# Kernel optimization log

Hardware: AMD Instinct MI355X
Metric: run time of the kernel (lower is better)

Reference implementation:

```python
import jax, jax.numpy as jnp
import numpy as np

NUM_HEADS = 12

def setup_inputs() -> dict:
    key = jax.random.key(0)
    ks = jax.random.split(key, 6)
    B, N, C, P = 16, 785, 768, 48
    return {
        "x": jax.random.normal(ks[0], (B, N, C), jnp.float32),
        "qkv_w": jax.random.normal(ks[1], (3 * C, C), jnp.float32) * 0.02,
        "pos_emb": jax.random.normal(ks[2], (N, N, P), jnp.float32) * 0.02,
        "pos_proj_w": jax.random.normal(ks[3], (NUM_HEADS, P), jnp.float32) * 0.02,
        "proj_w": jax.random.normal(ks[4], (C, C), jnp.float32) * 0.02,
        "proj_b": jnp.zeros((C,), jnp.float32),
    }

def reference(x, qkv_w, pos_emb, pos_proj_w, proj_w, proj_b):
    B, N, C = x.shape
    H = NUM_HEADS
    hd = C // H
    scale = hd ** -0.5
    # qkv projection: [B,N,3C] -> q,k,v each [B,H,N,hd]
    qkv = (x @ qkv_w.T).reshape(B, N, 3, H, hd)
    qkv = jnp.transpose(qkv, (2, 0, 3, 1, 4))
    q, k, v = qkv[0], qkv[1], qkv[2]
    # learned relative-position bias: [H,N,N]
    pos_score = jnp.einsum('nmp,hp->hnm', pos_emb, pos_proj_w)
    # attention scores: scale applied AFTER adding bias (matches original)
    attn = (jnp.einsum('bhnd,bhmd->bhnm', q, k) + pos_score[None]) * scale
    attn = jax.nn.softmax(attn, axis=-1)
    out = jnp.einsum('bhnm,bhmd->bhnd', attn, v)
    out = jnp.transpose(out, (0, 2, 1, 3)).reshape(B, N, C)
    return out @ proj_w.T + proj_b
```

## Files before the change

### kernel.cpp

```cpp
#include <hip/hip_runtime.h>
#include <hip/hip_fp16.h>

#define B_ 16
#define N_ 785
#define C_ 768
#define H_ 12
#define HD_ 64
#define P_ 48
#define M_ (B_*N_)
#define MPAD 12672
#define POSW 800
#define VTW  800
#define SCALE 0.125f

#define OFF_Q   0
#define OFF_K   9646080
#define OFF_VT  19292160
#define OFF_POS 29122560
#define OFF_XF  36658560
#define OFF_AO  OFF_XF
#define OFF_WQ  46390656
#define OFF_WP  48160128

struct __align__(16) Half8 { __half h[8]; };
typedef _Float16 half8_t __attribute__((ext_vector_type(8)));
typedef _Float16 half4_t __attribute__((ext_vector_type(4)));
typedef float f32x4 __attribute__((ext_vector_type(4)));

__device__ __forceinline__ void gl16(const void* g, void* l) {
    __builtin_amdgcn_global_load_lds(
        (const __attribute__((address_space(1))) void*)g,
        (__attribute__((address_space(3))) void*)l, 16, 0, 0);
}

#define NX4 2411520
#define NQ4 442368
#define NP4 147456
#define NTOT4 (NX4+NQ4+NP4)

__global__ __launch_bounds__(256) void convert_f16(
    const float* __restrict__ x, const float* __restrict__ wq,
    const float* __restrict__ wp, _Float16* __restrict__ xo,
    _Float16* __restrict__ wqo, _Float16* __restrict__ wpo)
{
    int i = blockIdx.x * 256 + threadIdx.x;
    const float4* s; _Float16* d; int o;
    if (i < NX4)            { s = (const float4*)x;  d = xo;  o = i; }
    else if (i < NX4 + NQ4) { s = (const float4*)wq; d = wqo; o = i - NX4; }
    else                    { s = (const float4*)wp; d = wpo; o = i - NX4 - NQ4; }
    float4 v = s[o];
    half4_t h = { (_Float16)v.x, (_Float16)v.y, (_Float16)v.z, (_Float16)v.w };
    *(half4_t*)&d[o * 4] = h;
}

__global__ __launch_bounds__(256) void qkv_gemm_mfma(
    const _Float16* __restrict__ A, const _Float16* __restrict__ Bw,
    __half* __restrict__ qh, __half* __restrict__ kh, __half* __restrict__ vth)
{
    __shared__ _Float16 Asl[128 * 32];
    __shared__ _Float16 Bsl[128 * 32];

    const int t  = threadIdx.x;
    const int w  = t >> 6;
    const int l  = t & 63;
    const int lr = l & 15;
    const int lg = l >> 4;
    const int wm = (w >> 1) * 64;
    const int wn = (w & 1) * 64;
    const int n0 = blockIdx.x * 128;
    const int m0 = blockIdx.y * 128;

    const int f1 = t + 256;
    const int ar0 = t >> 2,  ac0 = (t & 3) * 8;
    const int ar1 = f1 >> 2, ac1 = (f1 & 3) * 8;
    const _Float16* Ag0 = A  + (size_t)(m0 + ar0) * 768 + ac0;
    const _Float16* Ag1 = A  + (size_t)(m0 + ar1) * 768 + ac1;
    const _Float16* Bg0 = Bw + (size_t)(n0 + ar0) * 768 + ac0;
    const _Float16* Bg1 = Bw + (size_t)(n0 + ar1) * 768 + ac1;
    _Float16* Al0 = &Asl[t * 8];
    _Float16* Al1 = &Asl[f1 * 8];
    _Float16* Bl0 = &Bsl[t * 8];
    _Float16* Bl1 = &Bsl[f1 * 8];

    f32x4 acc[4][4];
    #pragma unroll
    for (int i = 0; i < 4; ++i)
        #pragma unroll
        for (int j = 0; j < 4; ++j) acc[i][j] = (f32x4){0.f, 0.f, 0.f, 0.f};

    for (int k0 = 0; k0 < 768; k0 += 32) {
        gl16(Ag0 + k0, Al0); gl16(Ag1 + k0, Al1);
        gl16(Bg0 + k0, Bl0); gl16(Bg1 + k0, Bl1);
        __syncthreads();
        half8_t af[4], bf[4];
        #pragma unroll
        for (int i = 0; i < 4; ++i)
            af[i] = *(const half8_t*)&Asl[(wm + i * 16 + lr) * 32 + lg * 8];
        #pragma unroll
        for (int j = 0; j < 4; ++j)
            bf[j] = *(const half8_t*)&Bsl[(wn + j * 16 + lr) * 32 + lg * 8];
        #pragma unroll
        for (int i = 0; i < 4; ++i)
            #pragma unroll
            for (int j = 0; j < 4; ++j)
                acc[i][j] = __builtin_amdgcn_mfma_f32_16x16x32_f16(af[i], bf[j], acc[i][j], 0, 0, 0);
        __syncthreads();
    }

    const int tsel  = blockIdx.x / 6;
    const int nbase = n0 - tsel * 768;
    #pragma unroll
    for (int i = 0; i < 4; ++i) {
        #pragma unroll
        for (int r = 0; r < 4; ++r) {
            const int m = m0 + wm + i * 16 + lg * 4 + r;
            if (m >= M_) continue;
            const int bb = m / N_, nn = m - bb * N_;
            #pragma unroll
            for (int j = 0; j < 4; ++j) {
                const int nsec = nbase + wn + j * 16 + lr;
                const int hh = nsec >> 6, dd = nsec & 63;
                const float v = acc[i][j][r];
                if (tsel == 0)
                    qh[((size_t)(bb * H_ + hh) * N_ + nn) * HD_ + dd] = __float2half(v * SCALE);
                else if (tsel == 1)
                    kh[((size_t)(bb * H_ + hh) * N_ + nn) * HD_ + dd] = __float2half(v);
                else
                    vth[((size_t)(bb * H_ + hh) * HD_ + dd) * VTW + nn] = __float2half(v);
            }
        }
    }
}

__global__ __launch_bounds__(256) void pos_kernel(
    const float* __restrict__ pe, const float* __restrict__ pw,
    __half* __restrict__ posh)
{
    __shared__ float W[H_][P_];
    const int t = threadIdx.x;
    for (int i = t; i < H_ * P_; i += 256) W[i / P_][i % P_] = pw[i];
    __syncthreads();
    int nm = blockIdx.x * 256 + t;
    if (nm >= N_ * N_) return;
    float e[48];
    const float4* src = (const float4*)(pe + (size_t)nm * 48);
    #pragma unroll
    for (int i = 0; i < 12; ++i) {
        float4 v = src[i];
        e[4*i] = v.x; e[4*i+1] = v.y; e[4*i+2] = v.z; e[4*i+3] = v.w;
    }
    int n = nm / N_, m = nm - n * N_;
    #pragma unroll
    for (int hh = 0; hh < H_; ++hh) {
        float s = 0.f;
        #pragma unroll
        for (int p = 0; p < 48; ++p) s = fmaf(e[p], W[hh][p], s);
        posh[((size_t)hh * N_ + n) * POSW + m] = __float2half(s * SCALE);
    }
}

__global__ __launch_bounds__(256) void attn_mfma(
    const _Float16* __restrict__ qh, const _Float16* __restrict__ kh,
    const _Float16* __restrict__ vt, const _Float16* __restrict__ posh,
    _Float16* __restrict__ aoh)
{
    __shared__ _Float16 Kl[64][72];
    __shared__ _Float16 Vl[64][72];
    __shared__ _Float16 Bl[64][72];
    __shared__ _Float16 Pl[4][16][72];

    const int t  = threadIdx.x;
    const int w  = t >> 6;
    const int l  = t & 63;
    const int lr = l & 15;
    const int lg = l >> 4;
    const int bh = blockIdx.y;
    const int h  = bh % H_;
    const int n0 = blockIdx.x * 64;

    const int qrow = n0 + w * 16 + lr;
    const int qrc  = qrow < N_ ? qrow : N_ - 1;
    const half8_t qf0 = *(const half8_t*)(qh + ((size_t)bh * N_ + qrc) * HD_ + lg * 8);
    const half8_t qf1 = *(const half8_t*)(qh + ((size_t)bh * N_ + qrc) * HD_ + 32 + lg * 8);

    f32x4 O0 = {0.f,0.f,0.f,0.f}, O1 = O0, O2 = O0, O3 = O0;
    float mr[4] = {-1e30f, -1e30f, -1e30f, -1e30f};
    float ls[4] = {0.f, 0.f, 0.f, 0.f};

    const int srow = t >> 2;
    const int scol = (t & 3) * 16;

    for (int c = 0; c < 13; ++c) {
        const int m0 = c * 64;
        {
            const int gm = (m0 + srow) < N_ ? (m0 + srow) : N_ - 1;
            const half8_t* ksrc = (const half8_t*)(kh + ((size_t)bh * N_ + gm) * HD_ + scol);
            *(half8_t*)&Kl[srow][scol]     = ksrc[0];
            *(half8_t*)&Kl[srow][scol + 8] = ksrc[1];
            const half8_t* vsrc = (const half8_t*)(vt + ((size_t)bh * HD_ + srow) * VTW + m0 + scol);
            *(half8_t*)&Vl[srow][scol]     = vsrc[0];
            *(half8_t*)&Vl[srow][scol + 8] = vsrc[1];
            const int gn = (n0 + srow) < N_ ? (n0 + srow) : N_ - 1;
            const half8_t* bsrc = (const half8_t*)(posh + ((size_t)h * N_ + gn) * POSW + m0 + scol);
            *(half8_t*)&Bl[srow][scol]     = bsrc[0];
            *(half8_t*)&Bl[srow][scol + 8] = bsrc[1];
        }
        __syncthreads();

        f32x4 s[4];
        #pragma unroll
        for (int ms = 0; ms < 4; ++ms) {
            half8_t k0 = *(const half8_t*)&Kl[ms * 16 + lr][lg * 8];
            half8_t k1 = *(const half8_t*)&Kl[ms * 16 + lr][32 + lg * 8];
            f32x4 acc = {0.f, 0.f, 0.f, 0.f};
            acc = __builtin_amdgcn_mfma_f32_16x16x32_f16(qf0, k0, acc, 0, 0, 0);
            acc = __builtin_amdgcn_mfma_f32_16x16x32_f16(qf1, k1, acc, 0, 0, 0);
            s[ms] = acc;
        }
        #pragma unroll
        for (int ms = 0; ms < 4; ++ms) {
            const bool valid = (m0 + ms * 16 + lr) < N_;
            #pragma unroll
            for (int r = 0; r < 4; ++r) {
                float b = (float)Bl[w * 16 + lg * 4 + r][ms * 16 + lr];
                s[ms][r] = valid ? (s[ms][r] + b) : -1e30f;
            }
        }
        float alpha[4];
        #pragma unroll
        for (int r = 0; r < 4; ++r) {
            float v = fmaxf(fmaxf(s[0][r], s[1][r]), fmaxf(s[2][r], s[3][r]));
            v = fmaxf(v, __shfl_xor(v, 1));
            v = fmaxf(v, __shfl_xor(v, 2));
            v = fmaxf(v, __shfl_xor(v, 4));
            v = fmaxf(v, __shfl_xor(v, 8));
            float mn = fmaxf(mr[r], v);
            alpha[r] = __expf(mr[r] - mn);
            mr[r] = mn;
        }
        float psum[4] = {0.f, 0.f, 0.f, 0.f};
        #pragma unroll
        for (int ms = 0; ms < 4; ++ms) {
            #pragma unroll
            for (int r = 0; r < 4; ++r) {
                float p = __expf(s[ms][r] - mr[r]);
                psum[r] += p;
                Pl[w][lg * 4 + r][ms * 16 + lr] = (_Float16)p;
            }
        }
        #pragma unroll
        for (int r = 0; r < 4; ++r) {
            float v = psum[r];
            v += __shfl_xor(v, 1);
            v += __shfl_xor(v, 2);
            v += __shfl_xor(v, 4);
            v += __shfl_xor(v, 8);
            ls[r] = ls[r] * alpha[r] + v;
            O0[r] *= alpha[r]; O1[r] *= alpha[r];
            O2[r] *= alpha[r]; O3[r] *= alpha[r];
        }
        const half8_t pa0 = *(const half8_t*)&Pl[w][lr][lg * 8];
        const half8_t pa1 = *(const half8_t*)&Pl[w][lr][32 + lg * 8];
        #pragma unroll
        for (int ds = 0; ds < 4; ++ds) {
            half8_t v0 = *(const half8_t*)&Vl[ds * 16 + lr][lg * 8];
            half8_t v1 = *(const half8_t*)&Vl[ds * 16 + lr][32 + lg * 8];
            f32x4& Od = (ds == 0 ? O0 : ds == 1 ? O1 : ds == 2 ? O2 : O3);
            Od = __builtin_amdgcn_mfma_f32_16x16x32_f16(pa0, v0, Od, 0, 0, 0);
            Od = __builtin_amdgcn_mfma_f32_16x16x32_f16(pa1, v1, Od, 0, 0, 0);
        }
        __syncthreads();
    }

    const int bb = bh / H_;
    #pragma unroll
    for (int r = 0; r < 4; ++r) {
        const int n = n0 + w * 16 + lg * 4 + r;
        if (n >= N_) continue;
        const float inv = 1.f / ls[r];
        _Float16* dst = aoh + ((size_t)(bb * N_ + n)) * C_ + h * HD_;
        dst[0 * 16 + lr] = (_Float16)(O0[r] * inv);
        dst[1 * 16 + lr] = (_Float16)(O1[r] * inv);
        dst[2 * 16 + lr] = (_Float16)(O2[r] * inv);
        dst[3 * 16 + lr] = (_Float16)(O3[r] * inv);
    }
}

__global__ __launch_bounds__(256) void proj_gemm_mfma(
    const _Float16* __restrict__ A, const _Float16* __restrict__ Bw,
    const float* __restrict__ bias, float* __restrict__ out)
{
    __shared__ _Float16 Asl[128 * 32];
    __shared__ _Float16 Bsl[128 * 32];

    const int t  = threadIdx.x;
    const int w  = t >> 6;
    const int l  = t & 63;
    const int lr = l & 15;
    const int lg = l >> 4;
    const int wm = (w >> 1) * 64;
    const int wn = (w & 1) * 64;
    const int n0 = blockIdx.x * 128;
    const int m0 = blockIdx.y * 128;

    const int f1 = t + 256;
    const int ar0 = t >> 2,  ac0 = (t & 3) * 8;
    const int ar1 = f1 >> 2, ac1 = (f1 & 3) * 8;
    const _Float16* Ag0 = A  + (size_t)(m0 + ar0) * 768 + ac0;
    const _Float16* Ag1 = A  + (size_t)(m0 + ar1) * 768 + ac1;
    const _Float16* Bg0 = Bw + (size_t)(n0 + ar0) * 768 + ac0;
    const _Float16* Bg1 = Bw + (size_t)(n0 + ar1) * 768 + ac1;
    _Float16* Al0 = &Asl[t * 8];
    _Float16* Al1 = &Asl[f1 * 8];
    _Float16* Bl0 = &Bsl[t * 8];
    _Float16* Bl1 = &Bsl[f1 * 8];

    f32x4 acc[4][4];
    #pragma unroll
    for (int i = 0; i < 4; ++i)
        #pragma unroll
        for (int j = 0; j < 4; ++j) acc[i][j] = (f32x4){0.f, 0.f, 0.f, 0.f};

    for (int k0 = 0; k0 < 768; k0 += 32) {
        gl16(Ag0 + k0, Al0); gl16(Ag1 + k0, Al1);
        gl16(Bg0 + k0, Bl0); gl16(Bg1 + k0, Bl1);
        __syncthreads();
        half8_t af[4], bf[4];
        #pragma unroll
        for (int i = 0; i < 4; ++i)
            af[i] = *(const half8_t*)&Asl[(wm + i * 16 + lr) * 32 + lg * 8];
        #pragma unroll
        for (int j = 0; j < 4; ++j)
            bf[j] = *(const half8_t*)&Bsl[(wn + j * 16 + lr) * 32 + lg * 8];
        #pragma unroll
        for (int i = 0; i < 4; ++i)
            #pragma unroll
            for (int j = 0; j < 4; ++j)
                acc[i][j] = __builtin_amdgcn_mfma_f32_16x16x32_f16(af[i], bf[j], acc[i][j], 0, 0, 0);
        __syncthreads();
    }

    float bj[4];
    #pragma unroll
    for (int j = 0; j < 4; ++j) bj[j] = bias[n0 + wn + j * 16 + lr];
    #pragma unroll
    for (int i = 0; i < 4; ++i) {
        #pragma unroll
        for (int r = 0; r < 4; ++r) {
            const int m = m0 + wm + i * 16 + lg * 4 + r;
            if (m >= M_) continue;
            #pragma unroll
            for (int j = 0; j < 4; ++j) {
                const int n = n0 + wn + j * 16 + lr;
                out[(size_t)m * 768 + n] = acc[i][j][r] + bj[j];
            }
        }
    }
}

extern "C" void kernel_launch(void* const* d_in, const int* in_sizes, int n_in,
                              void* d_out, int out_size, void* d_ws, size_t ws_size,
                              hipStream_t stream)
{
    const float* x     = (const float*)d_in[0];
    const float* qkv_w = (const float*)d_in[1];
    const float* pe    = (const float*)d_in[2];
    const float* pw    = (const float*)d_in[3];
    const float* pjw   = (const float*)d_in[4];
    const float* pjb   = (const float*)d_in[5];
    float* out = (float*)d_out;

    _Float16* wsh  = (_Float16*)d_ws;
    _Float16* qh   = wsh + OFF_Q;
    _Float16* kh   = wsh + OFF_K;
    _Float16* vth  = wsh + OFF_VT;
    _Float16* posh = wsh + OFF_POS;
    _Float16* xf   = wsh + OFF_XF;
    _Float16* aoh  = wsh + OFF_AO;
    _Float16* wqf  = wsh + OFF_WQ;
    _Float16* wpf  = wsh + OFF_WP;

    convert_f16<<<dim3(NTOT4 / 256), 256, 0, stream>>>(x, qkv_w, pjw, xf, wqf, wpf);
    qkv_gemm_mfma<<<dim3(18, 99), 256, 0, stream>>>(
        xf, wqf, (__half*)qh, (__half*)kh, (__half*)vth);
    pos_kernel<<<dim3((N_ * N_ + 255) / 256), 256, 0, stream>>>(pe, pw, (__half*)posh);
    attn_mfma<<<dim3(13, 192), 256, 0, stream>>>(qh, kh, vth, posh, aoh);
    proj_gemm_mfma<<<dim3(6, 99), 256, 0, stream>>>(aoh, wpf, pjb, out);
}
```

Before: 312.4 us.

## Restructure attention loop with register prefetch, transposed scores, exp2 and lazy rescale

The attention kernel now computes S transposed (K as the A operand), so probabilities land in registers already laid out as the A fragment for the PV MFMA. This removes the per-wave shared-memory P buffer and its round trip. The next K/V/bias tile is prefetched into registers while the current one is computed, and the softmax uses exp2 with log2e folded into the Q and pos-bias scale. The running max is only updated when it grows by more than 8, and s_setprio is raised around MFMA blocks in all GEMMs. The grid is flattened so batch varies fastest, which puts blocks that share the same pos-bias tile next to each other for L2 reuse. The cost is more register pressure, and the lazy rescale leans on fp32 headroom (p can reach 2^8 before rescaling).

```diff
diff --git a/kernel.cpp b/kernel.cpp
--- a/kernel.cpp
+++ b/kernel.cpp
@@ -8,19 +8,18 @@
 #define HD_ 64
 #define P_ 48
 #define M_ (B_*N_)
-#define MPAD 12672
-#define POSW 800
-#define VTW  800
-#define SCALE 0.125f
+#define POSW 832
+#define VTW  832
+#define SLOG2E 0.1803368801111244f
 
 #define OFF_Q   0
 #define OFF_K   9646080
 #define OFF_VT  19292160
-#define OFF_POS 29122560
-#define OFF_XF  36658560
+#define OFF_POS 29515776
+#define OFF_XF  37353216
 #define OFF_AO  OFF_XF
-#define OFF_WQ  46390656
-#define OFF_WP  48160128
+#define OFF_WQ  47085312
+#define OFF_WP  48854784
 
 struct __align__(16) Half8 { __half h[8]; };
 typedef _Float16 half8_t __attribute__((ext_vector_type(8)));
@@ -99,11 +98,13 @@
         #pragma unroll
         for (int j = 0; j < 4; ++j)
             bf[j] = *(const half8_t*)&Bsl[(wn + j * 16 + lr) * 32 + lg * 8];
+        __builtin_amdgcn_s_setprio(1);
         #pragma unroll
         for (int i = 0; i < 4; ++i)
             #pragma unroll
             for (int j = 0; j < 4; ++j)
                 acc[i][j] = __builtin_amdgcn_mfma_f32_16x16x32_f16(af[i], bf[j], acc[i][j], 0, 0, 0);
+        __builtin_amdgcn_s_setprio(0);
         __syncthreads();
     }
 
@@ -122,7 +123,7 @@
                 const int hh = nsec >> 6, dd = nsec & 63;
                 const float v = acc[i][j][r];
                 if (tsel == 0)
-                    qh[((size_t)(bb * H_ + hh) * N_ + nn) * HD_ + dd] = __float2half(v * SCALE);
+                    qh[((size_t)(bb * H_ + hh) * N_ + nn) * HD_ + dd] = __float2half(v * SLOG2E);
                 else if (tsel == 1)
                     kh[((size_t)(bb * H_ + hh) * N_ + nn) * HD_ + dd] = __float2half(v);
                 else
@@ -155,7 +156,7 @@
         float s = 0.f;
         #pragma unroll
         for (int p = 0; p < 48; ++p) s = fmaf(e[p], W[hh][p], s);
-        posh[((size_t)hh * N_ + n) * POSW + m] = __float2half(s * SCALE);
+        posh[((size_t)hh * N_ + n) * POSW + m] = __float2half(s * SLOG2E);
     }
 }
 
@@ -167,108 +168,152 @@
     __shared__ _Float16 Kl[64][72];
     __shared__ _Float16 Vl[64][72];
     __shared__ _Float16 Bl[64][72];
-    __shared__ _Float16 Pl[4][16][72];
 
     const int t  = threadIdx.x;
     const int w  = t >> 6;
     const int l  = t & 63;
     const int lr = l & 15;
     const int lg = l >> 4;
-    const int bh = blockIdx.y;
-    const int h  = bh % H_;
-    const int n0 = blockIdx.x * 64;
+
+    const int g   = blockIdx.x;
+    const int b   = g & 15;
+    const int grp = g >> 4;
+    const int qt  = grp / 12;
+    const int h   = grp - qt * 12;
+    const int bh  = b * H_ + h;
+    const int n0  = qt * 64;
 
     const int qrow = n0 + w * 16 + lr;
     const int qrc  = qrow < N_ ? qrow : N_ - 1;
-    const half8_t qf0 = *(const half8_t*)(qh + ((size_t)bh * N_ + qrc) * HD_ + lg * 8);
-    const half8_t qf1 = *(const half8_t*)(qh + ((size_t)bh * N_ + qrc) * HD_ + 32 + lg * 8);
+    const _Float16* qbase = qh + ((size_t)bh * N_ + qrc) * HD_;
+    const half8_t qf0 = *(const half8_t*)(qbase + lg * 8);
+    const half8_t qf1 = *(const half8_t*)(qbase + 32 + lg * 8);
 
     f32x4 O0 = {0.f,0.f,0.f,0.f}, O1 = O0, O2 = O0, O3 = O0;
-    float mr[4] = {-1e30f, -1e30f, -1e30f, -1e30f};
-    float ls[4] = {0.f, 0.f, 0.f, 0.f};
+    float m_run = -1e30f;
+    float l_run = 0.f;
 
     const int srow = t >> 2;
     const int scol = (t & 3) * 16;
+    const _Float16* kRow = kh + ((size_t)bh * N_) * HD_ + scol;
+    const _Float16* vRow = vt + ((size_t)bh * HD_ + srow) * VTW + scol;
+    const _Float16* bRow = posh + ((size_t)h * N_ + (n0 + srow < N_ ? n0 + srow : N_ - 1)) * POSW + scol;
+
+    half8_t rk0, rk1, rv0, rv1, rb0, rb1;
+    {
+        const int gm = srow < N_ ? srow : N_ - 1;
+        const half8_t* ks = (const half8_t*)(kRow + (size_t)gm * HD_);
+        rk0 = ks[0]; rk1 = ks[1];
+        const half8_t* vs = (const half8_t*)vRow;
+        rv0 = vs[0]; rv1 = vs[1];
+        const half8_t* bs = (const half8_t*)bRow;
+        rb0 = bs[0]; rb1 = bs[1];
+    }
 
     for (int c = 0; c < 13; ++c) {
-        const int m0 = c * 64;
-        {
-            const int gm = (m0 + srow) < N_ ? (m0 + srow) : N_ - 1;
-            const half8_t* ksrc = (const half8_t*)(kh + ((size_t)bh * N_ + gm) * HD_ + scol);
-            *(half8_t*)&Kl[srow][scol]     = ksrc[0];
-            *(half8_t*)&Kl[srow][scol + 8] = ksrc[1];
-            const half8_t* vsrc = (const half8_t*)(vt + ((size_t)bh * HD_ + srow) * VTW + m0 + scol);
-            *(half8_t*)&Vl[srow][scol]     = vsrc[0];
-            *(half8_t*)&Vl[srow][scol + 8] = vsrc[1];
-            const int gn = (n0 + srow) < N_ ? (n0 + srow) : N_ - 1;
-            const half8_t* bsrc = (const half8_t*)(posh + ((size_t)h * N_ + gn) * POSW + m0 + scol);
-            *(half8_t*)&Bl[srow][scol]     = bsrc[0];
-            *(half8_t*)&Bl[srow][scol + 8] = bsrc[1];
-        }
-        __syncthreads();
+        *(half8_t*)&Kl[srow][scol]     = rk0;
+        *(half8_t*)&Kl[srow][scol + 8] = rk1;
+        *(half8_t*)&Vl[srow][scol]     = rv0;
+        *(half8_t*)&Vl[srow][scol + 8] = rv1;
+        *(half8_t*)&Bl[srow][scol]     = rb0;
+        *(half8_t*)&Bl[srow][scol + 8] = rb1;
+        __syncthreads();
+
+        if (c < 12) {
+            const int m0n = (c + 1) * 64;
+            const int gm  = (m0n + srow) < N_ ? (m0n + srow) : N_ - 1;
+            const half8_t* ks = (const half8_t*)(kRow + (size_t)gm * HD_);
+            rk0 = ks[0]; rk1 = ks[1];
+            const half8_t* vs = (const half8_t*)(vRow + m0n);
+            rv0 = vs[0]; rv1 = vs[1];
+            const half8_t* bs = (const half8_t*)(bRow + m0n);
+            rb0 = bs[0]; rb1 = bs[1];
+        }
 
         f32x4 s[4];
+        __builtin_amdgcn_s_setprio(1);
         #pragma unroll
         for (int ms = 0; ms < 4; ++ms) {
             half8_t k0 = *(const half8_t*)&Kl[ms * 16 + lr][lg * 8];
             half8_t k1 = *(const half8_t*)&Kl[ms * 16 + lr][32 + lg * 8];
             f32x4 acc = {0.f, 0.f, 0.f, 0.f};
-            acc = __builtin_amdgcn_mfma_f32_16x16x32_f16(qf0, k0, acc, 0, 0, 0);
-            acc = __builtin_amdgcn_mfma_f32_16x16x32_f16(qf1, k1, acc, 0, 0, 0);
+            acc = __builtin_amdgcn_mfma_f32_16x16x32_f16(k0, qf0, acc, 0, 0, 0);
+            acc = __builtin_amdgcn_mfma_f32_16x16x32_f16(k1, qf1, acc, 0, 0, 0);
             s[ms] = acc;
         }
+        __builtin_amdgcn_s_setprio(0);
+
         #pragma unroll
         for (int ms = 0; ms < 4; ++ms) {
-            const bool valid = (m0 + ms * 16 + lr) < N_;
+            half4_t b4 = *(const half4_t*)&Bl[w * 16 + lr][ms * 16 + lg * 4];
+            s[ms][0] += (float)b4[0];
+            s[ms][1] += (float)b4[1];
+            s[ms][2] += (float)b4[2];
+            s[ms][3] += (float)b4[3];
+        }
+        if (c == 12) {
+            #pragma unroll
+            for (int ms = 0; ms < 4; ++ms)
+                #pragma unroll
+                for (int r = 0; r < 4; ++r)
+                    if (ms * 16 + lg * 4 + r >= 17) s[ms][r] = -1e30f;
+        }
+
+        float smax = fmaxf(fmaxf(fmaxf(s[0][0], s[0][1]), fmaxf(s[0][2], s[0][3])),
+                           fmaxf(fmaxf(s[1][0], s[1][1]), fmaxf(s[1][2], s[1][3])));
+        smax = fmaxf(smax, fmaxf(fmaxf(fmaxf(s[2][0], s[2][1]), fmaxf(s[2][2], s[2][3])),
+                                 fmaxf(fmaxf(s[3][0], s[3][1]), fmaxf(s[3][2], s[3][3]))));
+        smax = fmaxf(smax, __shfl_xor(smax, 16));
+        smax = fmaxf(smax, __shfl_xor(smax, 32));
+
+        if (__any(smax > m_run + 8.f)) {
+            const float mn    = fmaxf(m_run, smax);
+            const float alpha = exp2f(m_run - mn);
+            m_run = mn;
+            l_run *= alpha;
+            const float a0 = __shfl(alpha, lg * 4 + 0);
+            const float a1 = __shfl(alpha, lg * 4 + 1);
+            const float a2 = __shfl(alpha, lg * 4 + 2);
+            const float a3 = __shfl(alpha, lg * 4 + 3);
+            O0[0]*=a0; O0[1]*=a1; O0[2]*=a2; O0[3]*=a3;
+            O1[0]*=a0; O1[1]*=a1; O1[2]*=a2; O1[3]*=a3;
+            O2[0]*=a0; O2[1]*=a1; O2[2]*=a2; O2[3]*=a3;
+            O3[0]*=a0; O3[1]*=a1; O3[2]*=a2; O3[3]*=a3;
+        }
+
+        float p[4][4];
+        float psum = 0.f;
+        #pragma unroll
+        for (int ms = 0; ms < 4; ++ms)
             #pragma unroll
             for (int r = 0; r < 4; ++r) {
-                float b = (float)Bl[w * 16 + lg * 4 + r][ms * 16 + lr];
-                s[ms][r] = valid ? (s[ms][r] + b) : -1e30f;
+                p[ms][r] = exp2f(s[ms][r] - m_run);
+                psum += p[ms][r];
             }
-        }
-        float alpha[4];
-        #pragma unroll
-        for (int r = 0; r < 4; ++r) {
-            float v = fmaxf(fmaxf(s[0][r], s[1][r]), fmaxf(s[2][r], s[3][r]));
-            v = fmaxf(v, __shfl_xor(v, 1));
-            v = fmaxf(v, __shfl_xor(v, 2));
-            v = fmaxf(v, __shfl_xor(v, 4));
-            v = fmaxf(v, __shfl_xor(v, 8));
-            float mn = fmaxf(mr[r], v);
-            alpha[r] = __expf(mr[r] - mn);
-            mr[r] = mn;
-        }
-        float psum[4] = {0.f, 0.f, 0.f, 0.f};
-        #pragma unroll
-        for (int ms = 0; ms < 4; ++ms) {
-            #pragma unroll
-            for (int r = 0; r < 4; ++r) {
-                float p = __expf(s[ms][r] - mr[r]);
-                psum[r] += p;
-                Pl[w][lg * 4 + r][ms * 16 + lr] = (_Float16)p;
-            }
-        }
-        #pragma unroll
-        for (int r = 0; r < 4; ++r) {
-            float v = psum[r];
-            v += __shfl_xor(v, 1);
-            v += __shfl_xor(v, 2);
-            v += __shfl_xor(v, 4);
-            v += __shfl_xor(v, 8);
-            ls[r] = ls[r] * alpha[r] + v;
-            O0[r] *= alpha[r]; O1[r] *= alpha[r];
-            O2[r] *= alpha[r]; O3[r] *= alpha[r];
-        }
-        const half8_t pa0 = *(const half8_t*)&Pl[w][lr][lg * 8];
-        const half8_t pa1 = *(const half8_t*)&Pl[w][lr][32 + lg * 8];
+        psum += __shfl_xor(psum, 16);
+        psum += __shfl_xor(psum, 32);
+        l_run += psum;
+
+        half8_t pa0 = { (_Float16)p[0][0], (_Float16)p[0][1], (_Float16)p[0][2], (_Float16)p[0][3],
+                        (_Float16)p[1][0], (_Float16)p[1][1], (_Float16)p[1][2], (_Float16)p[1][3] };
+        half8_t pa1 = { (_Float16)p[2][0], (_Float16)p[2][1], (_Float16)p[2][2], (_Float16)p[2][3],
+                        (_Float16)p[3][0], (_Float16)p[3][1], (_Float16)p[3][2], (_Float16)p[3][3] };
+
+        __builtin_amdgcn_s_setprio(1);
         #pragma unroll
         for (int ds = 0; ds < 4; ++ds) {
-            half8_t v0 = *(const half8_t*)&Vl[ds * 16 + lr][lg * 8];
-            half8_t v1 = *(const half8_t*)&Vl[ds * 16 + lr][32 + lg * 8];
+            const _Float16* vr = &Vl[ds * 16 + lr][0];
+            half4_t v00 = *(const half4_t*)&vr[lg * 4];
+            half4_t v01 = *(const half4_t*)&vr[16 + lg * 4];
+            half4_t v10 = *(const half4_t*)&vr[32 + lg * 4];
+            half4_t v11 = *(const half4_t*)&vr[48 + lg * 4];
+            half8_t vf0 = __builtin_shufflevector(v00, v01, 0, 1, 2, 3, 4, 5, 6, 7);
+            half8_t vf1 = __builtin_shufflevector(v10, v11, 0, 1, 2, 3, 4, 5, 6, 7);
             f32x4& Od = (ds == 0 ? O0 : ds == 1 ? O1 : ds == 2 ? O2 : O3);
-            Od = __builtin_amdgcn_mfma_f32_16x16x32_f16(pa0, v0, Od, 0, 0, 0);
-            Od = __builtin_amdgcn_mfma_f32_16x16x32_f16(pa1, v1, Od, 0, 0, 0);
-        }
+            Od = __builtin_amdgcn_mfma_f32_16x16x32_f16(pa0, vf0, Od, 0, 0, 0);
+            Od = __builtin_amdgcn_mfma_f32_16x16x32_f16(pa1, vf1, Od, 0, 0, 0);
+        }
+        __builtin_amdgcn_s_setprio(0);
         __syncthreads();
     }
 
@@ -277,7 +322,8 @@
     for (int r = 0; r < 4; ++r) {
         const int n = n0 + w * 16 + lg * 4 + r;
         if (n >= N_) continue;
-        const float inv = 1.f / ls[r];
+        const float lv  = __shfl(l_run, lg * 4 + r);
+        const float inv = 1.f / lv;
         _Float16* dst = aoh + ((size_t)(bb * N_ + n)) * C_ + h * HD_;
         dst[0 * 16 + lr] = (_Float16)(O0[r] * inv);
         dst[1 * 16 + lr] = (_Float16)(O1[r] * inv);
@@ -332,11 +378,13 @@
         #pragma unroll
         for (int j = 0; j < 4; ++j)
             bf[j] = *(const half8_t*)&Bsl[(wn + j * 16 + lr) * 32 + lg * 8];
+        __builtin_amdgcn_s_setprio(1);
         #pragma unroll
         for (int i = 0; i < 4; ++i)
             #pragma unroll
             for (int j = 0; j < 4; ++j)
                 acc[i][j] = __builtin_amdgcn_mfma_f32_16x16x32_f16(af[i], bf[j], acc[i][j], 0, 0, 0);
+        __builtin_amdgcn_s_setprio(0);
         __syncthreads();
     }
 
@@ -384,6 +432,6 @@
     qkv_gemm_mfma<<<dim3(18, 99), 256, 0, stream>>>(
         xf, wqf, (__half*)qh, (__half*)kh, (__half*)vth);
     pos_kernel<<<dim3((N_ * N_ + 255) / 256), 256, 0, stream>>>(pe, pw, (__half*)posh);
-    attn_mfma<<<dim3(13, 192), 256, 0, stream>>>(qh, kh, vth, posh, aoh);
+    attn_mfma<<<dim3(13 * 12 * 16), 256, 0, stream>>>(qh, kh, vth, posh, aoh);
     proj_gemm_mfma<<<dim3(6, 99), 256, 0, stream>>>(aoh, wpf, pjb, out);
 }
```

After: 290.6 us. 7.0% less time.
